# Performance work log

Measured on AMD Instinct MI355X. Metric: run time of the kernel, lower is better.

Reference implementation:

```python
import jax, jax.numpy as jnp
import numpy as np

N_NODES = 20000
N_EDGES = 320000
N_GRAPHS = 256
F_IN = 128
HID = 512


def _xavier(key, shape, gain=1.0):
    fan_out, fan_in = shape
    a = gain * np.sqrt(6.0 / (fan_in + fan_out))
    return jax.random.uniform(key, shape, jnp.float32, -a, a)


def setup_inputs() -> dict:
    key = jax.random.key(0)
    ks = jax.random.split(key, 9)
    x = jax.random.normal(ks[0], (N_NODES, F_IN), jnp.float32)
    edge_index = jax.random.randint(ks[1], (2, N_EDGES), 0, N_NODES, dtype=jnp.int64)
    batch = jnp.sort(jax.random.randint(ks[2], (N_NODES,), 0, N_GRAPHS, dtype=jnp.int64))
    return {
        "x": x,
        "edge_index": edge_index,
        "batch": batch,
        "lin_W": _xavier(ks[3], (HID, F_IN)),
        "lin_b": jnp.zeros((HID,), jnp.float32),
        "W1": _xavier(ks[4], (HID, F_IN)),
        "b1": jnp.zeros((HID,), jnp.float32),
        "W2": _xavier(ks[5], (HID, HID)),
        "b2": jnp.zeros((HID,), jnp.float32),
        "W3": _xavier(ks[6], (HID, HID)),
        "b3": jnp.zeros((HID,), jnp.float32),
        "W4": _xavier(ks[7], (HID, HID)),
        "b4": jnp.zeros((HID,), jnp.float32),
    }


def _gcn_conv(x, W, b, src, dst, norm, n_nodes):
    # PyG GCNConv: h = x @ W.T; out_i = sum_j norm_ij * h_j (scatter over dst) + b
    h = x @ W.T
    msg = h[src] * norm[:, None]  # [E', H] gather + scale
    return jax.ops.segment_sum(msg, dst, num_segments=n_nodes) + b


def reference(x, edge_index, batch, lin_W, lin_b, W1, b1, W2, b2, W3, b3, W4, b4):
    n = x.shape[0]
    loop = jnp.arange(n, dtype=edge_index.dtype)
    src = jnp.concatenate([edge_index[0], loop])
    dst = jnp.concatenate([edge_index[1], loop])
    # symmetric normalization D^-1/2 (A+I) D^-1/2, degree = in-degree over dst
    deg = jax.ops.segment_sum(jnp.ones_like(src, dtype=x.dtype), dst, num_segments=n)
    dis = jnp.where(deg > 0, jax.lax.rsqrt(deg), 0.0)
    norm = dis[src] * dis[dst]

    x_l = x @ lin_W.T + lin_b  # dead code when act=None (kept for faithfulness)

    h1 = _gcn_conv(x, W1, b1, src, dst, norm, n)
    h2 = _gcn_conv(h1, W2, b2, src, dst, norm, n)
    h3 = _gcn_conv(h2, W3, b3, src, dst, norm, n)
    h4 = _gcn_conv(h3, W4, b4, src, dst, norm, n)
    h = jnp.concatenate([h1, h2, h3, h4], axis=1)  # [N, 4*HID]

    h_pooled = jax.ops.segment_max(h, batch, num_segments=N_GRAPHS)
    h_pos = (h > 0).astype(h.dtype)
    counts = jax.ops.segment_sum(jnp.ones((n,), h.dtype), batch, num_segments=N_GRAPHS)
    h_pos_pooled = jax.ops.segment_sum(h_pos, batch, num_segments=N_GRAPHS) / jnp.maximum(counts, 1.0)[:, None]
    return jnp.concatenate([h_pooled, h_pos_pooled], axis=1)  # [G, 8*HID]
```

## Files before the change

### kernel.cpp

```cpp
#include <hip/hip_runtime.h>
#include <cfloat>
#include <cmath>

#define F_IN 128
#define HID 512

typedef short bf16x8 __attribute__((ext_vector_type(8)));
typedef float f32x4 __attribute__((ext_vector_type(4)));

__device__ static inline void split_bf16(float v, short& hi, short& lo) {
    unsigned u = __float_as_uint(v);
    unsigned r = u + 0x7FFF + ((u >> 16) & 1);
    hi = (short)(r >> 16);
    float hf = __uint_as_float(((unsigned)(unsigned short)hi) << 16);
    float res = v - hf;
    unsigned u2 = __float_as_uint(res);
    unsigned r2 = u2 + 0x7FFF + ((u2 >> 16) & 1);
    lo = (short)(r2 >> 16);
}

__device__ static inline void gload_lds16(const void* g, void* l) {
    __builtin_amdgcn_global_load_lds(
        (const __attribute__((address_space(1))) unsigned int*)g,
        (__attribute__((address_space(3))) unsigned int*)l,
        16, 0, 0);
}


__global__ void zero_kernel(int* __restrict__ a, int n) {
    int i = blockIdx.x * blockDim.x + threadIdx.x;
    if (i < n) a[i] = 0;
}

__global__ void count_in_kernel(const int* __restrict__ dst, int* __restrict__ cnt, int E) {
    int e = blockIdx.x * blockDim.x + threadIdx.x;
    if (e < E) atomicAdd(&cnt[dst[e]], 1);
}

__global__ void scan_kernel(const int* __restrict__ cnt, int* __restrict__ offs, int n) {
    __shared__ int buf[1024];
    __shared__ int carry_s;
    if (threadIdx.x == 0) carry_s = 0;
    __syncthreads();
    for (int base = 0; base < n; base += 1024) {
        int i = base + threadIdx.x;
        int v = (i < n) ? cnt[i] : 0;
        buf[threadIdx.x] = v;
        __syncthreads();
        for (int s = 1; s < 1024; s <<= 1) {
            int t = (threadIdx.x >= s) ? buf[threadIdx.x - s] : 0;
            __syncthreads();
            buf[threadIdx.x] += t;
            __syncthreads();
        }
        int total = buf[1023];
        if (i < n) offs[i] = carry_s + buf[threadIdx.x] - v;
        __syncthreads();
        if (threadIdx.x == 0) carry_s += total;
        __syncthreads();
    }
    if (threadIdx.x == 0) offs[n] = carry_s;
}

__global__ void dis_starts_kernel(const int* __restrict__ offs, float* __restrict__ dis,
                                  const int* __restrict__ batch, int* __restrict__ starts,
                                  int n, int G) {
    int i = blockIdx.x * blockDim.x + threadIdx.x;
    if (i >= n) return;
    dis[i] = rsqrtf((float)(offs[i + 1] - offs[i] + 1));
    int b = batch[i];
    if (i == 0) {
        for (int g = 0; g <= b; g++) starts[g] = 0;
    } else {
        int bp = batch[i - 1];
        for (int g = bp + 1; g <= b; g++) starts[g] = i;
    }
    if (i == n - 1) {
        for (int g = b + 1; g <= G; g++) starts[g] = n;
    }
}

__global__ void fill_csr_kernel(const int* __restrict__ src, const int* __restrict__ dst,
                                const int* __restrict__ offs, int* __restrict__ cnt,
                                unsigned short* __restrict__ csr, int E) {
    int e = blockIdx.x * blockDim.x + threadIdx.x;
    if (e < E) {
        int d = dst[e];
        int p = atomicSub(&cnt[d], 1);
        csr[offs[d] + p - 1] = (unsigned short)src[e];
    }
}

__global__ void wconv_kernel(const float* __restrict__ W1, const float* __restrict__ W2,
                             const float* __restrict__ W3, const float* __restrict__ W4,
                             short* __restrict__ Whi, short* __restrict__ Wlo) {
    int i = blockIdx.x * blockDim.x + threadIdx.x;
    const int n1 = HID * F_IN, nk = HID * HID;
    float v;
    if (i < n1) v = W1[i];
    else if (i < n1 + nk) v = W2[i - n1];
    else if (i < n1 + 2 * nk) v = W3[i - n1 - nk];
    else if (i < n1 + 3 * nk) v = W4[i - n1 - 2 * nk];
    else return;
    short h, l;
    split_bf16(v, h, l);
    Whi[i] = h;
    Wlo[i] = l;
}

template <int F, int CHUNKS>
__global__ __launch_bounds__(64) void agg_phase_kernel(
    const float* __restrict__ H, const float* __restrict__ dis,
    const int* __restrict__ offs, const unsigned short* __restrict__ csr,
    short* __restrict__ Ahi, short* __restrict__ Alo, int n) {
    constexpr int LOWB = (CHUNKS >= 8) ? 8 : CHUNKS;
    constexpr int LB = (CHUNKS >= 8) ? 3 : 2;
    int blk = blockIdx.x;
    int c_lo = blk & (LOWB - 1);
    int rest = blk >> LB;
    int p = rest / n;
    int i = rest - p * n;
    int chunk = p * LOWB + c_lo;

    int tid = threadIdx.x;
    int half = tid >> 5;
    int lc = tid & 31;
    int col = chunk * 32 + lc;
    const float* Hc = H + col;

    float di = dis[i];
    float a = (half == 0) ? di * Hc[(size_t)i * F] : 0.0f;
    int e = offs[i], e1 = offs[i + 1];
    for (; e + 8 <= e1; e += 8) {
        int j0 = csr[e + half];
        int j1 = csr[e + 2 + half];
        int j2 = csr[e + 4 + half];
        int j3 = csr[e + 6 + half];
        float d0 = dis[j0], d1 = dis[j1], d2 = dis[j2], d3 = dis[j3];
        float r0 = Hc[(size_t)j0 * F], r1 = Hc[(size_t)j1 * F];
        float r2 = Hc[(size_t)j2 * F], r3 = Hc[(size_t)j3 * F];
        a += d0 * r0 + d1 * r1 + d2 * r2 + d3 * r3;
    }
    for (; e + half < e1; e += 2) {
        int j = csr[e + half];
        a += dis[j] * Hc[(size_t)j * F];
    }
    a += __shfl_xor(a, 32, 64);
    a *= di;
    if (half == 0) {
        short h, l;
        split_bf16(a, h, l);
        Ahi[(size_t)i * F + col] = h;
        Alo[(size_t)i * F + col] = l;
    }
}

__global__ __launch_bounds__(256) void gemm_mfma_kernel(
    const short* __restrict__ Ahi, const short* __restrict__ Alo,
    const short* __restrict__ Whi, const short* __restrict__ Wlo,
    const float* __restrict__ bias, float* __restrict__ C,
    int M, int K, int Nout, int MT, int MT8) {
    __shared__ __attribute__((aligned(16))) short lds[4][4096];

    int blk = blockIdx.x;
    int xcd = blk & 7;
    int r = blk >> 3;
    int n0t = r & 3;
    int mt = xcd * MT8 + (r >> 2);
    if (mt >= MT) return;
    int m0 = mt * 128, n0 = n0t * 128;

    int tid = threadIdx.x;
    int w = tid >> 6, l = tid & 63;
    int lrow = l & 15, lq = l >> 4;

    const short* gp = (w == 0) ? Ahi : (w == 1) ? Alo : (w == 2) ? Whi : Wlo;
    int base_mn = (w < 2) ? m0 : n0;

    f32x4 acc[4][4];
    #pragma unroll
    for (int i = 0; i < 4; i++)
        #pragma unroll
        for (int j = 0; j < 4; j++) acc[i][j] = (f32x4){0.f, 0.f, 0.f, 0.f};

    int wm = w >> 1, wn = w & 1;

    for (int k0 = 0; k0 < K; k0 += 32) {
        const short* gbase = gp + (size_t)(base_mn + lrow) * K + (k0 + lq * 8);
        #pragma unroll
        for (int s = 0; s < 8; s++) {
            gload_lds16(gbase + (size_t)s * 16 * K, &lds[w][s * 64 * 8]);
        }
        __syncthreads();

        bf16x8 ah[4], al[4], wh[4], wl[4];
        #pragma unroll
        for (int i = 0; i < 4; i++) {
            int sA = wm * 4 + i;
            ah[i] = *(const bf16x8*)&lds[0][(sA * 64 + l) * 8];
            al[i] = *(const bf16x8*)&lds[1][(sA * 64 + l) * 8];
            int sW = wn * 4 + i;
            wh[i] = *(const bf16x8*)&lds[2][(sW * 64 + l) * 8];
            wl[i] = *(const bf16x8*)&lds[3][(sW * 64 + l) * 8];
        }
        #pragma unroll
        for (int i = 0; i < 4; i++)
            #pragma unroll
            for (int j = 0; j < 4; j++) {
                acc[i][j] = __builtin_amdgcn_mfma_f32_16x16x32_bf16(ah[i], wh[j], acc[i][j], 0, 0, 0);
                acc[i][j] = __builtin_amdgcn_mfma_f32_16x16x32_bf16(ah[i], wl[j], acc[i][j], 0, 0, 0);
                acc[i][j] = __builtin_amdgcn_mfma_f32_16x16x32_bf16(al[i], wh[j], acc[i][j], 0, 0, 0);
            }
        __syncthreads();
    }

    #pragma unroll
    for (int j = 0; j < 4; j++) {
        int col = n0 + (wn * 4 + j) * 16 + lrow;
        float bv = bias[col];
        #pragma unroll
        for (int i = 0; i < 4; i++) {
            int mrow = m0 + (wm * 4 + i) * 16 + lq * 4;
            #pragma unroll
            for (int rr = 0; rr < 4; rr++) {
                int mm = mrow + rr;
                if (mm < M) C[(size_t)mm * Nout + col] = acc[i][j][rr] + bv;
            }
        }
    }
}

__global__ __launch_bounds__(64) void pool_kernel(
    const float* __restrict__ H, const int* __restrict__ starts,
    float* __restrict__ out, int layer) {
    int g = blockIdx.x;
    int c = blockIdx.y * 64 + threadIdx.x;
    int s = starts[g], e = starts[g + 1];
    float mx = -INFINITY;
    int pos = 0;
    #pragma unroll 4
    for (int n = s; n < e; n++) {
        float v = H[(size_t)n * HID + c];
        mx = fmaxf(mx, v);
        pos += (v > 0.0f) ? 1 : 0;
    }
    float cntf = fmaxf((float)(e - s), 1.0f);
    out[(size_t)g * (8 * HID) + layer * HID + c] = mx;
    out[(size_t)g * (8 * HID) + 4 * HID + layer * HID + c] = (float)pos / cntf;
}

extern "C" void kernel_launch(void* const* d_in, const int* in_sizes, int n_in,
                              void* d_out, int out_size, void* d_ws, size_t ws_size,
                              hipStream_t stream) {
    const float* x     = (const float*)d_in[0];
    const int*   eidx  = (const int*)d_in[1];
    const int*   batch = (const int*)d_in[2];
    const float* W1 = (const float*)d_in[5];
    const float* b1 = (const float*)d_in[6];
    const float* W2 = (const float*)d_in[7];
    const float* b2 = (const float*)d_in[8];
    const float* W3 = (const float*)d_in[9];
    const float* b3 = (const float*)d_in[10];
    const float* W4 = (const float*)d_in[11];
    const float* b4 = (const float*)d_in[12];
    float* out = (float*)d_out;

    const int N = in_sizes[0] / F_IN;
    const int E = in_sizes[1] / 2;
    const int G = out_size / (8 * HID);

    const int* src = eidx;
    const int* dst = eidx + E;

    const size_t nW = (size_t)HID * F_IN + 3 * (size_t)HID * HID;
    char* w = (char*)d_ws;
    short* Ahi = (short*)w; w += (size_t)N * HID * sizeof(short);
    short* Alo = (short*)w; w += (size_t)N * HID * sizeof(short);
    float* H   = (float*)w; w += (size_t)N * HID * sizeof(float);
    short* Whi = (short*)w; w += nW * sizeof(short);
    short* Wlo = (short*)w; w += nW * sizeof(short);
    int* offs  = (int*)w;   w += (size_t)(N + 4) * sizeof(int);
    unsigned short* csr = (unsigned short*)w; w += (size_t)E * sizeof(unsigned short);
    int* cnt   = (int*)w;   w += (size_t)N * sizeof(int);
    float* dis = (float*)w; w += (size_t)N * sizeof(float);
    int* starts = (int*)w;  w += (size_t)(G + 1) * sizeof(int);

    const size_t wo1 = 0;
    const size_t wo2 = (size_t)HID * F_IN;
    const size_t wo3 = wo2 + (size_t)HID * HID;
    const size_t wo4 = wo3 + (size_t)HID * HID;

    const int TB = 256;
    zero_kernel<<<(N + TB - 1) / TB, TB, 0, stream>>>(cnt, N);
    count_in_kernel<<<(E + TB - 1) / TB, TB, 0, stream>>>(dst, cnt, E);
    scan_kernel<<<1, 1024, 0, stream>>>(cnt, offs, N);
    dis_starts_kernel<<<(N + TB - 1) / TB, TB, 0, stream>>>(offs, dis, batch, starts, N, G);
    fill_csr_kernel<<<(E + TB - 1) / TB, TB, 0, stream>>>(src, dst, offs, cnt, csr, E);
    wconv_kernel<<<((int)nW + TB - 1) / TB, TB, 0, stream>>>(W1, W2, W3, W4, Whi, Wlo);

    const int MT = (N + 127) / 128;
    const int MT8 = (MT + 7) / 8;
    const int gemm_blocks = 8 * MT8 * 4;
    dim3 pool_grid(G, HID / 64);

    agg_phase_kernel<F_IN, 4><<<N * 4, 64, 0, stream>>>(x, dis, offs, csr, Ahi, Alo, N);
    gemm_mfma_kernel<<<gemm_blocks, 256, 0, stream>>>(Ahi, Alo, Whi + wo1, Wlo + wo1, b1, H,
                                                      N, F_IN, HID, MT, MT8);
    pool_kernel<<<pool_grid, 64, 0, stream>>>(H, starts, out, 0);

    const size_t wos[3] = {wo2, wo3, wo4};
    const float* bs_[3] = {b2, b3, b4};
    for (int ll = 0; ll < 3; ll++) {
        agg_phase_kernel<HID, 16><<<N * 16, 64, 0, stream>>>(H, dis, offs, csr, Ahi, Alo, N);
        gemm_mfma_kernel<<<gemm_blocks, 256, 0, stream>>>(Ahi, Alo, Whi + wos[ll], Wlo + wos[ll], bs_[ll], H,
                                                          N, HID, HID, MT, MT8);
        pool_kernel<<<pool_grid, 64, 0, stream>>>(H, starts, out, ll + 1);
    }
}
```

Measured before the change: 763.1 us.

## Pre-scale features by D^-1/2 in GEMM epilogue and batch CSR indices via shuffles

The GEMM epilogue now stores rows already multiplied by dis[row], and layer 1 input is pre-scaled by a new xscale kernel. The aggregation gather therefore no longer loads dis[j] per neighbour. It also loads up to 64 CSR indices at once per wave and broadcasts them with shuffles, unrolling 8 gathers per half. Pooling undoes the scaling with a precomputed sqrt(deg) per node, which adds a multiply and a rounding difference for the max and sign tests.

```diff
diff --git a/kernel.cpp b/kernel.cpp
--- a/kernel.cpp
+++ b/kernel.cpp
@@ -63,11 +63,14 @@
 }
 
 __global__ void dis_starts_kernel(const int* __restrict__ offs, float* __restrict__ dis,
+                                  float* __restrict__ rdis,
                                   const int* __restrict__ batch, int* __restrict__ starts,
                                   int n, int G) {
     int i = blockIdx.x * blockDim.x + threadIdx.x;
     if (i >= n) return;
-    dis[i] = rsqrtf((float)(offs[i + 1] - offs[i] + 1));
+    float degp1 = (float)(offs[i + 1] - offs[i] + 1);
+    dis[i] = rsqrtf(degp1);
+    rdis[i] = sqrtf(degp1);
     int b = batch[i];
     if (i == 0) {
         for (int g = 0; g <= b; g++) starts[g] = 0;
@@ -108,45 +111,68 @@
     Wlo[i] = l;
 }
 
+__global__ void xscale_kernel(const float* __restrict__ x, const float* __restrict__ dis,
+                              float* __restrict__ xs, int total) {
+    int i = blockIdx.x * blockDim.x + threadIdx.x;
+    if (i < total) xs[i] = x[i] * dis[i >> 7];
+}
+
 template <int F, int CHUNKS>
-__global__ __launch_bounds__(64) void agg_phase_kernel(
-    const float* __restrict__ H, const float* __restrict__ dis,
+__global__ __launch_bounds__(64) void agg_gather_kernel(
+    const float* __restrict__ Hs, const float* __restrict__ dis,
     const int* __restrict__ offs, const unsigned short* __restrict__ csr,
     short* __restrict__ Ahi, short* __restrict__ Alo, int n) {
     constexpr int LOWB = (CHUNKS >= 8) ? 8 : CHUNKS;
     constexpr int LB = (CHUNKS >= 8) ? 3 : 2;
+    constexpr int PHASES = CHUNKS / LOWB;
     int blk = blockIdx.x;
     int c_lo = blk & (LOWB - 1);
     int rest = blk >> LB;
-    int p = rest / n;
-    int i = rest - p * n;
+    int p = 0, i = rest;
+    if (PHASES > 1 && rest >= n) { p = 1; i = rest - n; }
     int chunk = p * LOWB + c_lo;
 
     int tid = threadIdx.x;
     int half = tid >> 5;
     int lc = tid & 31;
     int col = chunk * 32 + lc;
-    const float* Hc = H + col;
-
-    float di = dis[i];
-    float a = (half == 0) ? di * Hc[(size_t)i * F] : 0.0f;
-    int e = offs[i], e1 = offs[i + 1];
-    for (; e + 8 <= e1; e += 8) {
-        int j0 = csr[e + half];
-        int j1 = csr[e + 2 + half];
-        int j2 = csr[e + 4 + half];
-        int j3 = csr[e + 6 + half];
-        float d0 = dis[j0], d1 = dis[j1], d2 = dis[j2], d3 = dis[j3];
-        float r0 = Hc[(size_t)j0 * F], r1 = Hc[(size_t)j1 * F];
-        float r2 = Hc[(size_t)j2 * F], r3 = Hc[(size_t)j3 * F];
-        a += d0 * r0 + d1 * r1 + d2 * r2 + d3 * r3;
-    }
-    for (; e + half < e1; e += 2) {
-        int j = csr[e + half];
-        a += dis[j] * Hc[(size_t)j * F];
+    const float* Hc = Hs + col;
+
+    int e0 = offs[i], e1 = offs[i + 1];
+    float a = (half == 0) ? Hc[(size_t)i * F] : 0.0f;
+
+    for (int w = e0; w < e1; w += 64) {
+        int cnt = e1 - w; if (cnt > 64) cnt = 64;
+        int idx = 0;
+        if (tid < cnt) idx = csr[w + tid];
+        int tb = 0;
+        for (; tb + 16 <= cnt; tb += 16) {
+            int j0 = __shfl(idx, tb + half,      64);
+            int j1 = __shfl(idx, tb + half + 2,  64);
+            int j2 = __shfl(idx, tb + half + 4,  64);
+            int j3 = __shfl(idx, tb + half + 6,  64);
+            int j4 = __shfl(idx, tb + half + 8,  64);
+            int j5 = __shfl(idx, tb + half + 10, 64);
+            int j6 = __shfl(idx, tb + half + 12, 64);
+            int j7 = __shfl(idx, tb + half + 14, 64);
+            float r0 = Hc[(size_t)j0 * F];
+            float r1 = Hc[(size_t)j1 * F];
+            float r2 = Hc[(size_t)j2 * F];
+            float r3 = Hc[(size_t)j3 * F];
+            float r4 = Hc[(size_t)j4 * F];
+            float r5 = Hc[(size_t)j5 * F];
+            float r6 = Hc[(size_t)j6 * F];
+            float r7 = Hc[(size_t)j7 * F];
+            a += ((r0 + r1) + (r2 + r3)) + ((r4 + r5) + (r6 + r7));
+        }
+        for (int t = tb; t < cnt; t += 2) {
+            int tt = t + half;
+            int j = __shfl(idx, (tt < 64) ? tt : 0, 64);
+            if (tt < cnt) a += Hc[(size_t)j * F];
+        }
     }
     a += __shfl_xor(a, 32, 64);
-    a *= di;
+    a *= dis[i];
     if (half == 0) {
         short h, l;
         split_bf16(a, h, l);
@@ -158,7 +184,8 @@
 __global__ __launch_bounds__(256) void gemm_mfma_kernel(
     const short* __restrict__ Ahi, const short* __restrict__ Alo,
     const short* __restrict__ Whi, const short* __restrict__ Wlo,
-    const float* __restrict__ bias, float* __restrict__ C,
+    const float* __restrict__ bias, const float* __restrict__ dis,
+    float* __restrict__ Hs,
     int M, int K, int Nout, int MT, int MT8) {
     __shared__ __attribute__((aligned(16))) short lds[4][4096];
 
@@ -214,6 +241,17 @@
         __syncthreads();
     }
 
+    float dv[4][4];
+    #pragma unroll
+    for (int i = 0; i < 4; i++) {
+        int mrow = m0 + (wm * 4 + i) * 16 + lq * 4;
+        #pragma unroll
+        for (int rr = 0; rr < 4; rr++) {
+            int mm = mrow + rr;
+            dv[i][rr] = (mm < M) ? dis[mm] : 0.0f;
+        }
+    }
+
     #pragma unroll
     for (int j = 0; j < 4; j++) {
         int col = n0 + (wn * 4 + j) * 16 + lrow;
@@ -224,14 +262,15 @@
             #pragma unroll
             for (int rr = 0; rr < 4; rr++) {
                 int mm = mrow + rr;
-                if (mm < M) C[(size_t)mm * Nout + col] = acc[i][j][rr] + bv;
+                if (mm < M) Hs[(size_t)mm * Nout + col] = dv[i][rr] * (acc[i][j][rr] + bv);
             }
         }
     }
 }
 
 __global__ __launch_bounds__(64) void pool_kernel(
-    const float* __restrict__ H, const int* __restrict__ starts,
+    const float* __restrict__ Hs, const float* __restrict__ rdis,
+    const int* __restrict__ starts,
     float* __restrict__ out, int layer) {
     int g = blockIdx.x;
     int c = blockIdx.y * 64 + threadIdx.x;
@@ -240,7 +279,7 @@
     int pos = 0;
     #pragma unroll 4
     for (int n = s; n < e; n++) {
-        float v = H[(size_t)n * HID + c];
+        float v = Hs[(size_t)n * HID + c] * rdis[n];
         mx = fmaxf(mx, v);
         pos += (v > 0.0f) ? 1 : 0;
     }
@@ -276,13 +315,15 @@
     char* w = (char*)d_ws;
     short* Ahi = (short*)w; w += (size_t)N * HID * sizeof(short);
     short* Alo = (short*)w; w += (size_t)N * HID * sizeof(short);
-    float* H   = (float*)w; w += (size_t)N * HID * sizeof(float);
+    float* Hs  = (float*)w; w += (size_t)N * HID * sizeof(float);
+    float* xs  = (float*)w; w += (size_t)N * F_IN * sizeof(float);
     short* Whi = (short*)w; w += nW * sizeof(short);
     short* Wlo = (short*)w; w += nW * sizeof(short);
     int* offs  = (int*)w;   w += (size_t)(N + 4) * sizeof(int);
     unsigned short* csr = (unsigned short*)w; w += (size_t)E * sizeof(unsigned short);
     int* cnt   = (int*)w;   w += (size_t)N * sizeof(int);
     float* dis = (float*)w; w += (size_t)N * sizeof(float);
+    float* rdis = (float*)w; w += (size_t)N * sizeof(float);
     int* starts = (int*)w;  w += (size_t)(G + 1) * sizeof(int);
 
     const size_t wo1 = 0;
@@ -294,26 +335,27 @@
     zero_kernel<<<(N + TB - 1) / TB, TB, 0, stream>>>(cnt, N);
     count_in_kernel<<<(E + TB - 1) / TB, TB, 0, stream>>>(dst, cnt, E);
     scan_kernel<<<1, 1024, 0, stream>>>(cnt, offs, N);
-    dis_starts_kernel<<<(N + TB - 1) / TB, TB, 0, stream>>>(offs, dis, batch, starts, N, G);
+    dis_starts_kernel<<<(N + TB - 1) / TB, TB, 0, stream>>>(offs, dis, rdis, batch, starts, N, G);
     fill_csr_kernel<<<(E + TB - 1) / TB, TB, 0, stream>>>(src, dst, offs, cnt, csr, E);
     wconv_kernel<<<((int)nW + TB - 1) / TB, TB, 0, stream>>>(W1, W2, W3, W4, Whi, Wlo);
+    xscale_kernel<<<(N * F_IN + TB - 1) / TB, TB, 0, stream>>>(x, dis, xs, N * F_IN);
 
     const int MT = (N + 127) / 128;
     const int MT8 = (MT + 7) / 8;
     const int gemm_blocks = 8 * MT8 * 4;
     dim3 pool_grid(G, HID / 64);
 
-    agg_phase_kernel<F_IN, 4><<<N * 4, 64, 0, stream>>>(x, dis, offs, csr, Ahi, Alo, N);
-    gemm_mfma_kernel<<<gemm_blocks, 256, 0, stream>>>(Ahi, Alo, Whi + wo1, Wlo + wo1, b1, H,
+    agg_gather_kernel<F_IN, 4><<<N * 4, 64, 0, stream>>>(xs, dis, offs, csr, Ahi, Alo, N);
+    gemm_mfma_kernel<<<gemm_blocks, 256, 0, stream>>>(Ahi, Alo, Whi + wo1, Wlo + wo1, b1, dis, Hs,
                                                       N, F_IN, HID, MT, MT8);
-    pool_kernel<<<pool_grid, 64, 0, stream>>>(H, starts, out, 0);
+    pool_kernel<<<pool_grid, 64, 0, stream>>>(Hs, rdis, starts, out, 0);
 
     const size_t wos[3] = {wo2, wo3, wo4};
     const float* bs_[3] = {b2, b3, b4};
     for (int ll = 0; ll < 3; ll++) {
-        agg_phase_kernel<HID, 16><<<N * 16, 64, 0, stream>>>(H, dis, offs, csr, Ahi, Alo, N);
-        gemm_mfma_kernel<<<gemm_blocks, 256, 0, stream>>>(Ahi, Alo, Whi + wos[ll], Wlo + wos[ll], bs_[ll], H,
+        agg_gather_kernel<HID, 16><<<N * 16, 64, 0, stream>>>(Hs, dis, offs, csr, Ahi, Alo, N);
+        gemm_mfma_kernel<<<gemm_blocks, 256, 0, stream>>>(Ahi, Alo, Whi + wos[ll], Wlo + wos[ll], bs_[ll], dis, Hs,
                                                           N, HID, HID, MT, MT8);
-        pool_kernel<<<pool_grid, 64, 0, stream>>>(H, starts, out, ll + 1);
-    }
-}
+        pool_kernel<<<pool_grid, 64, 0, stream>>>(Hs, rdis, starts, out, ll + 1);
+    }
+}
```

Result: slower. 783.5 us (+2.7%).
